# Optimization experiments

Hardware: AMD Instinct MI355X
Metric: run time of the kernel (lower is better)

Reference implementation:

```python
import jax, jax.numpy as jnp
import numpy as np

HIDDEN = 2560
N_HEADS = 32
HEAD_DIM = HIDDEN // N_HEADS  # 80
ROPE_PCT = 0.25
ROT = int(HEAD_DIM * ROPE_PCT)  # 20
THETA = 10000.0


def setup_inputs() -> dict:
    key = jax.random.key(0)
    ks = jax.random.split(key, 6)
    B, S = 2, 2048
    hidden_states = jax.random.normal(ks[0], (B, S, HIDDEN), dtype=jnp.float32)
    attention_mask = jnp.ones((B, S), dtype=jnp.float32)  # unused in no-cache path
    position_ids = jnp.tile(jnp.arange(S, dtype=jnp.int32)[None, :], (B, 1))
    scale = 1.0 / np.sqrt(HIDDEN)
    Wq = jax.random.normal(ks[1], (HIDDEN, HIDDEN), dtype=jnp.float32) * scale
    Wk = jax.random.normal(ks[2], (HIDDEN, HIDDEN), dtype=jnp.float32) * scale
    Wv = jax.random.normal(ks[3], (HIDDEN, HIDDEN), dtype=jnp.float32) * scale
    Wo = jax.random.normal(ks[4], (HIDDEN, HIDDEN), dtype=jnp.float32) * scale
    return {"hidden_states": hidden_states, "attention_mask": attention_mask,
            "position_ids": position_ids, "Wq": Wq, "Wk": Wk, "Wv": Wv, "Wo": Wo}


def _rotate_half(x):
    x1, x2 = jnp.split(x, 2, axis=-1)
    return jnp.concatenate([-x2, x1], axis=-1)


def _rope_cos_sin(position_ids, dtype):
    # inv_freq over rotary dims
    inv_freq = 1.0 / (THETA ** (jnp.arange(0, ROT, 2, dtype=jnp.float32) / ROT))
    pos = position_ids.astype(jnp.float32)  # [B,S]
    freqs = pos[..., None] * inv_freq[None, None, :]  # [B,S,ROT/2]
    emb = jnp.concatenate([freqs, freqs], axis=-1)    # [B,S,ROT]
    cos = jnp.cos(emb)[:, None, :, :].astype(dtype)   # [B,1,S,ROT]
    sin = jnp.sin(emb)[:, None, :, :].astype(dtype)
    return cos, sin


def reference(hidden_states, attention_mask, position_ids, Wq, Wk, Wv, Wo):
    B, S, H = hidden_states.shape
    dtype = hidden_states.dtype
    # projections: [B,S,H] -> [B,nh,S,hd]
    def split_heads(x):
        return x.reshape(B, S, N_HEADS, HEAD_DIM).transpose(0, 2, 1, 3)
    q = split_heads(hidden_states @ Wq)
    k = split_heads(hidden_states @ Wk)
    v = split_heads(hidden_states @ Wv)

    # partial RoPE on first ROT dims
    cos, sin = _rope_cos_sin(position_ids, dtype)
    q_rot, q_pass = q[..., :ROT], q[..., ROT:]
    k_rot, k_pass = k[..., :ROT], k[..., ROT:]
    q_rot = q_rot * cos + _rotate_half(q_rot) * sin
    k_rot = k_rot * cos + _rotate_half(k_rot) * sin
    q = jnp.concatenate([q_rot, q_pass], axis=-1)
    k = jnp.concatenate([k_rot, k_pass], axis=-1)

    # causal attention (no KV cache -> is_causal=True SDPA path)
    scale = 1.0 / np.sqrt(HEAD_DIM)
    scores = jnp.einsum("bhqd,bhkd->bhqk", q, k) * scale
    causal = jnp.tril(jnp.ones((S, S), dtype=bool))
    scores = jnp.where(causal[None, None, :, :], scores, jnp.finfo(jnp.float32).min)
    probs = jax.nn.softmax(scores.astype(jnp.float32), axis=-1).astype(dtype)
    attn = jnp.einsum("bhqk,bhkd->bhqd", probs, v)
    attn = attn.transpose(0, 2, 1, 3).reshape(B, S, H)
    return attn @ Wo
```

## Files before the change

### kernel.cpp

```cpp
#include <hip/hip_runtime.h>
#include <stdint.h>

typedef unsigned short u16;
typedef __bf16 bf16x8 __attribute__((ext_vector_type(8)));
typedef float floatx4 __attribute__((ext_vector_type(4)));

#define HIDDEN 2560
#define NHEADS 32
#define HD 80
#define SEQ 2048
#define BATCH 2
#define MROWS (BATCH*SEQ)
#define QB 64

__device__ __forceinline__ float bf2f(uint32_t bits) {
    return __uint_as_float(bits << 16);
}
__device__ __forceinline__ u16 f2bf_bits(float f) {
    uint32_t x = __float_as_uint(f);
    uint32_t r = (x + 0x7fffu + ((x >> 16) & 1u)) >> 16;
    return (u16)r;
}
__device__ __forceinline__ floatx4 mk4(float x) {
    return (floatx4){x, x, x, x};
}
__device__ __forceinline__ floatx4 exp4(floatx4 a) {
    floatx4 r;
#pragma unroll
    for (int i = 0; i < 4; i++) r[i] = __expf(a[i]);
    return r;
}
__device__ __forceinline__ void gload16(const u16* g, u16* l) {
    __builtin_amdgcn_global_load_lds(
        (const __attribute__((address_space(1))) uint32_t*)g,
        (__attribute__((address_space(3))) uint32_t*)l, 16, 0, 0);
}

__global__ __launch_bounds__(256) void split_x(const float* __restrict__ in,
                                               u16* __restrict__ hi,
                                               u16* __restrict__ lo,
                                               float scale) {
    size_t i4 = (size_t)blockIdx.x * 256 + threadIdx.x;
    float4 v = ((const float4*)in)[i4];
    float f[4] = {v.x * scale, v.y * scale, v.z * scale, v.w * scale};
    u16 h[4], l[4];
#pragma unroll
    for (int j = 0; j < 4; j++) {
        h[j] = f2bf_bits(f[j]);
        l[j] = f2bf_bits(f[j] - bf2f(h[j]));
    }
    ((uint2*)hi)[i4] = *(uint2*)h;
    ((uint2*)lo)[i4] = *(uint2*)l;
}

__global__ __launch_bounds__(256) void split_wt(const float* __restrict__ in,
                                                u16* __restrict__ outh,
                                                u16* __restrict__ outl) {
    __shared__ float t[64][65];
    int k0 = blockIdx.x * 64;
    int n0 = blockIdx.y * 64;
    int tid = threadIdx.x;
    int rr = tid >> 4;
    int c4 = (tid & 15) * 4;
#pragma unroll
    for (int it = 0; it < 4; it++) {
        int row = it * 16 + rr;
        float4 v = *(const float4*)&in[(size_t)(k0 + row) * HIDDEN + n0 + c4];
        t[row][c4 + 0] = v.x; t[row][c4 + 1] = v.y;
        t[row][c4 + 2] = v.z; t[row][c4 + 3] = v.w;
    }
    __syncthreads();
#pragma unroll
    for (int it = 0; it < 4; it++) {
        int row = it * 16 + rr;
        float f[4] = { t[c4 + 0][row], t[c4 + 1][row], t[c4 + 2][row], t[c4 + 3][row] };
        u16 h[4], l[4];
#pragma unroll
        for (int j = 0; j < 4; j++) {
            h[j] = f2bf_bits(f[j]);
            l[j] = f2bf_bits(f[j] - bf2f(h[j]));
        }
        size_t o = (size_t)(n0 + row) * HIDDEN + k0 + c4;
        *(uint2*)&outh[o] = *(uint2*)h;
        *(uint2*)&outl[o] = *(uint2*)l;
    }
}

__global__ __launch_bounds__(256) void gemm_bt2(const u16* __restrict__ Ah,
                                                const u16* __restrict__ Al,
                                                const u16* __restrict__ Bh,
                                                const u16* __restrict__ Bl,
                                                float* __restrict__ C) {
    __shared__ u16 lAh[128 * 32];
    __shared__ u16 lAl[128 * 32];
    __shared__ u16 lBh[128 * 32];
    __shared__ u16 lBl[128 * 32];
    const int K = HIDDEN;
    int tid  = threadIdx.x;
    int lane = tid & 63;
    int wave = tid >> 6;
    int wr = wave >> 1, wc = wave & 1;
    int m0 = blockIdx.y * 128, n0 = blockIdx.x * 128;
    int lr = lane & 15, lq = lane >> 4;

    int srow = wave * 32 + (lane >> 2);
    int scol = ((lane & 3) ^ ((lane >> 3) & 3)) * 8;
    const u16* gAh = Ah + (size_t)(m0 + srow) * K + scol;
    const u16* gAl = Al + (size_t)(m0 + srow) * K + scol;
    const u16* gBh = Bh + (size_t)(n0 + srow) * K + scol;
    const u16* gBl = Bl + (size_t)(n0 + srow) * K + scol;
    const size_t q1 = (size_t)16 * K;
    u16* dAh = &lAh[(wave * 32) * 32];
    u16* dAl = &lAl[(wave * 32) * 32];
    u16* dBh = &lBh[(wave * 32) * 32];
    u16* dBl = &lBl[(wave * 32) * 32];

    floatx4 acc[4][4];
#pragma unroll
    for (int i = 0; i < 4; i++)
#pragma unroll
        for (int j = 0; j < 4; j++)
            acc[i][j] = mk4(0.f);

    int swz = (lr >> 1) & 3;
    int rsl = (lq ^ swz) * 8;

    for (int k0 = 0; k0 < K; k0 += 32) {
        gload16(gAh + k0, dAh);  gload16(gAh + q1 + k0, dAh + 16 * 32);
        gload16(gAl + k0, dAl);  gload16(gAl + q1 + k0, dAl + 16 * 32);
        gload16(gBh + k0, dBh);  gload16(gBh + q1 + k0, dBh + 16 * 32);
        gload16(gBl + k0, dBl);  gload16(gBl + q1 + k0, dBl + 16 * 32);
        __syncthreads();
        bf16x8 ah[4], al[4], bh[4], bl[4];
#pragma unroll
        for (int i = 0; i < 4; i++) {
            int ra = (wr * 64 + i * 16 + lr) * 32 + rsl;
            int rb = (wc * 64 + i * 16 + lr) * 32 + rsl;
            ah[i] = *(const bf16x8*)&lAh[ra];
            al[i] = *(const bf16x8*)&lAl[ra];
            bh[i] = *(const bf16x8*)&lBh[rb];
            bl[i] = *(const bf16x8*)&lBl[rb];
        }
#pragma unroll
        for (int i = 0; i < 4; i++)
#pragma unroll
            for (int j = 0; j < 4; j++) {
                acc[i][j] = __builtin_amdgcn_mfma_f32_16x16x32_bf16(ah[i], bh[j], acc[i][j], 0, 0, 0);
                acc[i][j] = __builtin_amdgcn_mfma_f32_16x16x32_bf16(ah[i], bl[j], acc[i][j], 0, 0, 0);
                acc[i][j] = __builtin_amdgcn_mfma_f32_16x16x32_bf16(al[i], bh[j], acc[i][j], 0, 0, 0);
            }
        __syncthreads();
    }
#pragma unroll
    for (int i = 0; i < 4; i++) {
        int rowb = m0 + wr * 64 + i * 16 + lq * 4;
#pragma unroll
        for (int j = 0; j < 4; j++) {
            int col = n0 + wc * 64 + j * 16 + lr;
#pragma unroll
            for (int r = 0; r < 4; r++)
                C[(size_t)(rowb + r) * HIDDEN + col] = acc[i][j][r];
        }
    }
}

__global__ __launch_bounds__(256) void rope_k(float* __restrict__ Qb, float* __restrict__ Kb,
                                              const int* __restrict__ pos_ids) {
    int idx = blockIdx.x * 256 + threadIdx.x;
    int row = idx >> 5;
    int h   = idx & 31;
    float pos = (float)pos_ids[row];
    size_t base = (size_t)row * HIDDEN + h * HD;
    float* q = Qb + base;
    float* k = Kb + base;
#pragma unroll
    for (int i = 0; i < 10; i++) {
        float freq = pos * exp2f(-1.3287712379549449f * (float)i);
        float sn, cs;
        sincosf(freq, &sn, &cs);
        float q1 = q[i], q2 = q[i + 10];
        q[i]      = q1 * cs - q2 * sn;
        q[i + 10] = q2 * cs + q1 * sn;
        float k1 = k[i], k2 = k[i + 10];
        k[i]      = k1 * cs - k2 * sn;
        k[i + 10] = k2 * cs + k1 * sn;
    }
}

__global__ __launch_bounds__(256) void vtrans(const float* __restrict__ Vb,
                                              u16* __restrict__ Vth,
                                              u16* __restrict__ Vtl) {
    __shared__ float t[64][81];
    int bh = blockIdx.x; int b = bh >> 5, h = bh & 31;
    int s0 = blockIdx.y * 64;
    int tid = threadIdx.x;
    for (int idx = tid; idx < 64 * 20; idx += 256) {
        int s = idx / 20, c = idx % 20;
        float4 v = *(const float4*)&Vb[(size_t)(b * SEQ + s0 + s) * HIDDEN + h * HD + c * 4];
        t[s][c * 4 + 0] = v.x; t[s][c * 4 + 1] = v.y;
        t[s][c * 4 + 2] = v.z; t[s][c * 4 + 3] = v.w;
    }
    __syncthreads();
    for (int idx = tid; idx < 80 * 16; idx += 256) {
        int d = idx >> 4, ch = idx & 15;
        int t2 = ch >> 3, e = ch & 7, a = e >> 1, h2 = e & 1;
        int srck = t2 * 32 + 16 * h2 + 4 * a;
        int dstc = t2 * 32 + 8 * a + 4 * h2;
        u16 hh[4], ll[4];
#pragma unroll
        for (int j = 0; j < 4; j++) {
            float f = t[srck + j][d];
            hh[j] = f2bf_bits(f);
            ll[j] = f2bf_bits(f - bf2f(hh[j]));
        }
        size_t o = ((size_t)bh * HD + d) * SEQ + s0 + dstc;
        *(uint2*)&Vth[o] = *(uint2*)hh;
        *(uint2*)&Vtl[o] = *(uint2*)ll;
    }
}

__global__ __launch_bounds__(256, 4) void attn_mfma(const u16* __restrict__ Qh_,
                                                 const u16* __restrict__ Ql_,
                                                 const u16* __restrict__ Kh_,
                                                 const u16* __restrict__ Kl_,
                                                 const u16* __restrict__ Vth_,
                                                 const u16* __restrict__ Vtl_,
                                                 u16* __restrict__ Oh_,
                                                 u16* __restrict__ Ol_) {
    __shared__ u16 lds[20480];

    int tid = threadIdx.x;
    int lane = tid & 63, w = tid >> 6;
    int lr = lane & 15, lq = lane >> 4;
    int bh = blockIdx.x; int b = bh >> 5, h = bh & 31;
    int qblk = (gridDim.y - 1) - blockIdx.y;
    int q0 = qblk * QB;
    size_t rowbase = (size_t)b * SEQ;
    size_t hoff = (size_t)h * HD;

    bf16x8 qh[2], ql[2], qta;
    for (int idx = tid; idx < 1280; idx += 256) {
        int buf = idx >= 640; int e = idx - buf * 640;
        int r = e / 10, c = e % 10;
        const u16* src = (buf ? Ql_ : Qh_) +
            (rowbase + q0 + r) * HIDDEN + hoff + c * 8;
        *(int4*)&lds[buf * 6656 + r * 104 + c * 8] = *(const int4*)src;
    }
    __syncthreads();
    {
        int tba = (lq >> 1) ? 6656 : 0;
        int tcol = 64 + (lq & 1) * 8;
        int lrow = w * 16 + lr;
#pragma unroll
        for (int c = 0; c < 2; c++) {
            qh[c] = *(const bf16x8*)&lds[lrow * 104 + c * 32 + lq * 8];
            ql[c] = *(const bf16x8*)&lds[6656 + lrow * 104 + c * 32 + lq * 8];
        }
        qta = *(const bf16x8*)&lds[tba + lrow * 104 + tcol];
    }
    __syncthreads();

    floatx4 acc[5];
    float mrow = -3.0e38f, lsum = 0.f;
#pragma unroll
    for (int nt = 0; nt < 5; nt++) acc[nt] = mk4(0.f);

    int ntiles = 2 * qblk + 2;
    int qw0 = q0 + w * 16;

    int k0RowOff = (lane >> 3) * HIDDEN + (((lane & 7) ^ (lane >> 3)) * 8);
    int k1RowOff = (lane >> 1) * HIDDEN + 64 + (lane & 1) * 8;
    int vRowOff  = (lane >> 2) * SEQ + ((((lane & 3) ^ ((lane >> 3) & 3))) * 8);
    const u16* kSrc = (w & 1 ? Kl_ : Kh_) + rowbase * HIDDEN + hoff;
    const u16* vSrc = (w == 3 ? Vtl_ : Vth_) + (size_t)bh * HD * SEQ;

    auto stage = [&](int t, int bsel) {
        int k0 = t * 32;
        u16* B = lds + bsel * 10240;
        if (w < 2) {
            const u16* kb = kSrc + (size_t)k0 * HIDDEN;
            u16* d0 = B + w * 2048;
#pragma unroll
            for (int j = 0; j < 4; j++)
                gload16(kb + (size_t)j * 8 * HIDDEN + k0RowOff, d0 + j * 512);
            gload16(kb + k1RowOff, B + 4096 + w * 512);
        } else {
            const u16* vb = vSrc + k0;
            u16* d0 = B + 5120 + (w == 3 ? 2560 : 0);
#pragma unroll
            for (int j = 0; j < 5; j++)
                gload16(vb + (size_t)j * 16 * SEQ + vRowOff, d0 + j * 512);
        }
    };

    int ks0 = ((lq) ^ (lr & 7)) * 8;
    int ks1 = ((4 + lq) ^ (lr & 7)) * 8;
    int k1off  = (lq >> 1) * 512 + (lq & 1) * 8;
    int k1offb = ((lq >> 1) ^ 1) * 512 + (lq & 1) * 8;
    int vsl = (lq ^ ((lr >> 1) & 3)) * 8;

    stage(0, 0);

    for (int t = 0; t < ntiles; t++) {
        int k0 = t * 32;
        __syncthreads();
        if (t + 1 < ntiles) stage(t + 1, (t + 1) & 1);
        u16* B = lds + (t & 1) * 10240;
        if (k0 <= qw0 + 15) {
            u16* bK0h = B;
            u16* bK0l = B + 2048;
            u16* bK1  = B + 4096;
            u16* bVh  = B + 5120;
            u16* bVl  = B + 7680;
            __builtin_amdgcn_s_setprio(1);
            floatx4 s[2];
#pragma unroll
            for (int st = 0; st < 2; st++) {
                int krow = st * 16 + lr;
                bf16x8 kh0 = *(const bf16x8*)&bK0h[krow * 64 + ks0];
                bf16x8 kh1 = *(const bf16x8*)&bK0h[krow * 64 + ks1];
                bf16x8 kl0 = *(const bf16x8*)&bK0l[krow * 64 + ks0];
                bf16x8 kl1 = *(const bf16x8*)&bK0l[krow * 64 + ks1];
                bf16x8 k1f  = *(const bf16x8*)&bK1[krow * 16 + k1off];
                bf16x8 k1fb = *(const bf16x8*)&bK1[krow * 16 + k1offb];
                floatx4 sv = mk4(0.f);
                sv = __builtin_amdgcn_mfma_f32_16x16x32_bf16(kh0, qh[0], sv, 0, 0, 0);
                sv = __builtin_amdgcn_mfma_f32_16x16x32_bf16(kl0, qh[0], sv, 0, 0, 0);
                sv = __builtin_amdgcn_mfma_f32_16x16x32_bf16(kh0, ql[0], sv, 0, 0, 0);
                sv = __builtin_amdgcn_mfma_f32_16x16x32_bf16(kh1, qh[1], sv, 0, 0, 0);
                sv = __builtin_amdgcn_mfma_f32_16x16x32_bf16(kl1, qh[1], sv, 0, 0, 0);
                sv = __builtin_amdgcn_mfma_f32_16x16x32_bf16(kh1, ql[1], sv, 0, 0, 0);
                sv = __builtin_amdgcn_mfma_f32_16x16x32_bf16(k1f,  qta, sv, 0, 0, 0);
                sv = __builtin_amdgcn_mfma_f32_16x16x32_bf16(k1fb, qta, sv, 0, 0, 0);
                s[st] = sv;
            }
            if (k0 + 31 > qw0) {
                int qmy = qw0 + lr - k0 - lq * 4;
#pragma unroll
                for (int r = 0; r < 4; r++) {
                    s[0][r] = (r <= qmy)      ? s[0][r] : -3.0e38f;
                    s[1][r] = (16 + r <= qmy) ? s[1][r] : -3.0e38f;
                }
            }
            float rm = fmaxf(fmaxf(fmaxf(s[0][0], s[0][1]), fmaxf(s[0][2], s[0][3])),
                             fmaxf(fmaxf(s[1][0], s[1][1]), fmaxf(s[1][2], s[1][3])));
            rm = fmaxf(rm, __shfl_xor(rm, 16));
            rm = fmaxf(rm, __shfl_xor(rm, 32));
            int need = rm > mrow + 8.f;
            if (__any(need)) {
                float mnew = fmaxf(mrow, rm);
                float alpha = __expf(mrow - mnew);
                mrow = mnew;
                lsum *= alpha;
                float at[4];
#pragma unroll
                for (int r = 0; r < 4; r++) at[r] = __shfl(alpha, lq * 4 + r);
#pragma unroll
                for (int nt = 0; nt < 5; nt++)
#pragma unroll
                    for (int r = 0; r < 4; r++) acc[nt][r] *= at[r];
            }
            floatx4 p0 = exp4(s[0] - mk4(mrow));
            floatx4 p1 = exp4(s[1] - mk4(mrow));
            floatx4 ps = p0 + p1;
            float rs = ps[0] + ps[1] + ps[2] + ps[3];
            rs += __shfl_xor(rs, 16);
            rs += __shfl_xor(rs, 32);
            lsum += rs;
            bf16x8 pa;
            pa[0] = (__bf16)p0[0]; pa[1] = (__bf16)p0[1];
            pa[2] = (__bf16)p0[2]; pa[3] = (__bf16)p0[3];
            pa[4] = (__bf16)p1[0]; pa[5] = (__bf16)p1[1];
            pa[6] = (__bf16)p1[2]; pa[7] = (__bf16)p1[3];
#pragma unroll
            for (int nt = 0; nt < 5; nt++) {
                bf16x8 vh = *(const bf16x8*)&bVh[(nt * 16 + lr) * 32 + vsl];
                bf16x8 vl = *(const bf16x8*)&bVl[(nt * 16 + lr) * 32 + vsl];
                acc[nt] = __builtin_amdgcn_mfma_f32_16x16x32_bf16(pa, vh, acc[nt], 0, 0, 0);
                acc[nt] = __builtin_amdgcn_mfma_f32_16x16x32_bf16(pa, vl, acc[nt], 0, 0, 0);
            }
            __builtin_amdgcn_s_setprio(0);
        }
    }
    {
        float il = 1.f / lsum;
        float inv[4];
#pragma unroll
        for (int r = 0; r < 4; r++) inv[r] = __shfl(il, lq * 4 + r);
#pragma unroll
        for (int nt = 0; nt < 5; nt++) {
#pragma unroll
            for (int r = 0; r < 4; r++) {
                float o = acc[nt][r] * inv[r];
                u16 hh = f2bf_bits(o);
                u16 ll = f2bf_bits(o - bf2f(hh));
                size_t row = rowbase + qw0 + lq * 4 + r;
                Oh_[row * HIDDEN + hoff + nt * 16 + lr] = hh;
                Ol_[row * HIDDEN + hoff + nt * 16 + lr] = ll;
            }
        }
    }
}

extern "C" void kernel_launch(void* const* d_in, const int* in_sizes, int n_in,
                              void* d_out, int out_size, void* d_ws, size_t ws_size,
                              hipStream_t stream) {
    const float* hidden = (const float*)d_in[0];
    const int* pos    = (const int*)d_in[2];
    const float* Wq   = (const float*)d_in[3];
    const float* Wk   = (const float*)d_in[4];
    const float* Wv   = (const float*)d_in[5];
    const float* Wo   = (const float*)d_in[6];

    const size_t NQ = (size_t)MROWS * HIDDEN;
    float* ws = (float*)d_ws;
    float* Qb = ws;
    float* Kb = ws + NQ;
    float* Vb = ws + 2 * NQ;
    u16* Ah  = (u16*)(ws + 3 * NQ);
    u16* Al  = Ah + NQ;
    u16* WTh = Al + NQ;
    u16* WTl = WTh + (size_t)HIDDEN * HIDDEN;
    u16* Vth = Ah;
    u16* Vtl = Al;
    u16* Qh  = (u16*)Vb;
    u16* Ql  = Qh + NQ;
    u16* Kh  = (u16*)Qb;
    u16* Kl  = Kh + NQ;
    u16* Oh  = (u16*)Kb;
    u16* Ol  = Oh + NQ;

    const float SC = 0.11180339887498949f;

    dim3 blk(256);
    dim3 wgrid(HIDDEN / 64, HIDDEN / 64);
    dim3 ggrid(HIDDEN / 128, MROWS / 128);

    split_x<<<dim3(NQ / 1024), blk, 0, stream>>>(hidden, Ah, Al, 1.f);
    split_wt<<<wgrid, blk, 0, stream>>>(Wq, WTh, WTl);
    gemm_bt2<<<ggrid, blk, 0, stream>>>(Ah, Al, WTh, WTl, Qb);
    split_wt<<<wgrid, blk, 0, stream>>>(Wk, WTh, WTl);
    gemm_bt2<<<ggrid, blk, 0, stream>>>(Ah, Al, WTh, WTl, Kb);
    split_wt<<<wgrid, blk, 0, stream>>>(Wv, WTh, WTl);
    gemm_bt2<<<ggrid, blk, 0, stream>>>(Ah, Al, WTh, WTl, Vb);
    rope_k<<<dim3(MROWS * NHEADS / 256), blk, 0, stream>>>(Qb, Kb, pos);
    vtrans<<<dim3(BATCH * NHEADS, SEQ / 64), blk, 0, stream>>>(Vb, Vth, Vtl);
    split_x<<<dim3(NQ / 1024), blk, 0, stream>>>(Qb, Qh, Ql, SC);
    split_x<<<dim3(NQ / 1024), blk, 0, stream>>>(Kb, Kh, Kl, 1.f);
    attn_mfma<<<dim3(BATCH * NHEADS, SEQ / QB), blk, 0, stream>>>(Qh, Ql, Kh, Kl,
                                                                  Vth, Vtl, Oh, Ol);
    split_wt<<<wgrid, blk, 0, stream>>>(Wo, WTh, WTl);
    gemm_bt2<<<ggrid, blk, 0, stream>>>(Oh, Ol, WTh, WTl, (float*)d_out);
}
```

Before: 1.174 ms.

## Double-buffer LDS in split-bf16 GEMM and remap workgroups across XCDs

The split-bf16 GEMM now keeps two LDS buffers and issues the global-to-LDS load for the next K tile before computing the current one. This removes one barrier per iteration and overlaps memory traffic with the MFMA work. It also remaps block indices so that consecutive tiles land on the same XCD, which should improve L2 reuse. The cost is twice the LDS footprint (64KB), which may lower occupancy. The remap assumes the grid size is divisible by 8.

```diff
diff --git a/kernel.cpp b/kernel.cpp
--- a/kernel.cpp
+++ b/kernel.cpp
@@ -91,17 +91,19 @@
                                                 const u16* __restrict__ Bh,
                                                 const u16* __restrict__ Bl,
                                                 float* __restrict__ C) {
-    __shared__ u16 lAh[128 * 32];
-    __shared__ u16 lAl[128 * 32];
-    __shared__ u16 lBh[128 * 32];
-    __shared__ u16 lBl[128 * 32];
+    __shared__ u16 lds[2 * 16384];
     const int K = HIDDEN;
     int tid  = threadIdx.x;
     int lane = tid & 63;
     int wave = tid >> 6;
     int wr = wave >> 1, wc = wave & 1;
-    int m0 = blockIdx.y * 128, n0 = blockIdx.x * 128;
     int lr = lane & 15, lq = lane >> 4;
+
+    int nwgx = gridDim.x;
+    int orig = blockIdx.y * nwgx + blockIdx.x;
+    int cpx  = (nwgx * gridDim.y) >> 3;
+    int wg   = (orig & 7) * cpx + (orig >> 3);
+    int n0 = (wg % nwgx) * 128, m0 = (wg / nwgx) * 128;
 
     int srow = wave * 32 + (lane >> 2);
     int scol = ((lane & 3) ^ ((lane >> 3) & 3)) * 8;
@@ -110,10 +112,7 @@
     const u16* gBh = Bh + (size_t)(n0 + srow) * K + scol;
     const u16* gBl = Bl + (size_t)(n0 + srow) * K + scol;
     const size_t q1 = (size_t)16 * K;
-    u16* dAh = &lAh[(wave * 32) * 32];
-    u16* dAl = &lAl[(wave * 32) * 32];
-    u16* dBh = &lBh[(wave * 32) * 32];
-    u16* dBl = &lBl[(wave * 32) * 32];
+    int dso = wave * 1024;
 
     floatx4 acc[4][4];
 #pragma unroll
@@ -125,21 +124,29 @@
     int swz = (lr >> 1) & 3;
     int rsl = (lq ^ swz) * 8;
 
-    for (int k0 = 0; k0 < K; k0 += 32) {
-        gload16(gAh + k0, dAh);  gload16(gAh + q1 + k0, dAh + 16 * 32);
-        gload16(gAl + k0, dAl);  gload16(gAl + q1 + k0, dAl + 16 * 32);
-        gload16(gBh + k0, dBh);  gload16(gBh + q1 + k0, dBh + 16 * 32);
-        gload16(gBl + k0, dBl);  gload16(gBl + q1 + k0, dBl + 16 * 32);
+    auto stage = [&](int k0, int bsel) {
+        u16* Bf = lds + bsel * 16384 + dso;
+        gload16(gAh + k0, Bf);          gload16(gAh + q1 + k0, Bf + 512);
+        gload16(gAl + k0, Bf + 4096);   gload16(gAl + q1 + k0, Bf + 4608);
+        gload16(gBh + k0, Bf + 8192);   gload16(gBh + q1 + k0, Bf + 8704);
+        gload16(gBl + k0, Bf + 12288);  gload16(gBl + q1 + k0, Bf + 12800);
+    };
+
+    const int NT = K / 32;
+    stage(0, 0);
+    for (int t = 0; t < NT; t++) {
         __syncthreads();
+        if (t + 1 < NT) stage((t + 1) * 32, (t + 1) & 1);
+        u16* Bc = lds + (t & 1) * 16384;
         bf16x8 ah[4], al[4], bh[4], bl[4];
 #pragma unroll
         for (int i = 0; i < 4; i++) {
             int ra = (wr * 64 + i * 16 + lr) * 32 + rsl;
             int rb = (wc * 64 + i * 16 + lr) * 32 + rsl;
-            ah[i] = *(const bf16x8*)&lAh[ra];
-            al[i] = *(const bf16x8*)&lAl[ra];
-            bh[i] = *(const bf16x8*)&lBh[rb];
-            bl[i] = *(const bf16x8*)&lBl[rb];
+            ah[i] = *(const bf16x8*)&Bc[ra];
+            al[i] = *(const bf16x8*)&Bc[4096 + ra];
+            bh[i] = *(const bf16x8*)&Bc[8192 + rb];
+            bl[i] = *(const bf16x8*)&Bc[12288 + rb];
         }
 #pragma unroll
         for (int i = 0; i < 4; i++)
@@ -149,7 +156,6 @@
                 acc[i][j] = __builtin_amdgcn_mfma_f32_16x16x32_bf16(ah[i], bl[j], acc[i][j], 0, 0, 0);
                 acc[i][j] = __builtin_amdgcn_mfma_f32_16x16x32_bf16(al[i], bh[j], acc[i][j], 0, 0, 0);
             }
-        __syncthreads();
     }
 #pragma unroll
     for (int i = 0; i < 4; i++) {
```

Result: no change. 1.177 ms (+0.3%).
